# Kernel optimization log

Measured on AMD Instinct MI355X. Metric: run time of the kernel, lower is better.

## Reference

```python
import jax, jax.numpy as jnp
import numpy as np

N, E, D, H, L = 4096, 131072, 2048, 4, 2  # nodes, edges, embed_dim, heads, layers
HD = D // H


def setup_inputs() -> dict:
    key = jax.random.key(0)
    ks = jax.random.split(key, 11)
    s = 0.02
    feats = jax.random.normal(ks[0], (N, D), jnp.float32)
    edge_index = jax.random.randint(ks[1], (E, 2), 0, N, dtype=jnp.int32)
    # per-layer linear params, stored as [in, out] so y = x @ W + b (== torch x @ W.T + b)
    Wq = jax.random.normal(ks[2], (L, D, D), jnp.float32) * s
    Wk = jax.random.normal(ks[3], (L, D, D), jnp.float32) * s
    Wv = jax.random.normal(ks[4], (L, D, D), jnp.float32) * s
    Wo = jax.random.normal(ks[5], (L, D, D), jnp.float32) * s
    bq = jnp.zeros((L, D), jnp.float32)
    bk = jnp.zeros((L, D), jnp.float32)
    bv = jnp.zeros((L, D), jnp.float32)
    bo = jnp.zeros((L, D), jnp.float32)
    return dict(feats=feats, Wq=Wq, bq=bq, Wk=Wk, bk=bk, Wv=Wv, bv=bv,
                Wo=Wo, bo=bo, edge_index=edge_index)


def _gnn_forward(feats, Wq, bq, Wk, bk, Wv, bv, Wo, bo, row, col):
    n = feats.shape[0]
    # dense edge mask [1, N, N] (masked_fill where mask == 0 -> -10000)
    mask = jnp.zeros((n, n), bool).at[row, col].set(True)[None]
    scale = 1.0 / jnp.sqrt(jnp.asarray(HD, feats.dtype))
    x = feats
    for l in range(L):
        q = (x @ Wq[l] + bq[l]).reshape(n, H, HD).transpose(1, 0, 2)  # [H,N,d]
        k = (x @ Wk[l] + bk[l]).reshape(n, H, HD).transpose(1, 0, 2)
        v = (x @ Wv[l] + bv[l]).reshape(n, H, HD).transpose(1, 0, 2)
        scores = jnp.einsum('hnd,hmd->hnm', q, k) * scale          # [H,N,N]
        scores = jnp.where(mask, scores, jnp.asarray(-10000.0, scores.dtype))
        attn = jax.nn.softmax(scores, axis=-1)                      # [H,N,N]
        se = attn[:, row, col]                                      # [H,E] gather per-edge
        out_e = se[:, :, None] * v[:, col]                          # [H,E,d]
        agg = jax.vmap(lambda o: jax.ops.segment_sum(o, row, num_segments=n))(out_e)  # [H,N,d]
        x = agg.transpose(1, 0, 2).reshape(n, H * HD) @ Wo[l] + bo[l]
    return x


def reference(feats, Wq, bq, Wk, bk, Wv, bv, Wo, bo, edge_index):
    row, col = edge_index[:, 0], edge_index[:, 1]
    return _gnn_forward(feats, Wq, bq, Wk, bk, Wv, bv, Wo, bo, row, col)
```

## Files before the change

kernel.cpp:

```cpp
#include <hip/hip_runtime.h>
#include <hip/hip_bf16.h>

typedef unsigned short u16;
typedef unsigned int u32;
typedef short bf16x8 __attribute__((ext_vector_type(8)));
typedef float f32x4 __attribute__((ext_vector_type(4)));
typedef unsigned short u16x4 __attribute__((ext_vector_type(4)));
typedef unsigned short u16x8 __attribute__((ext_vector_type(8)));
typedef float f32x4v __attribute__((ext_vector_type(4)));

#define NN 4096
#define DD 2048
#define HH 4
#define HDIM 512
#define EE 131072
#define NB 512
#define EBS 256
#define QS 6144

__device__ __forceinline__ float bf2f(u16 x) {
    return __uint_as_float(((u32)x) << 16);
}
__device__ __forceinline__ u16 f2bf(float f) {
    u32 u = __float_as_uint(f);
    u += 0x7fffu + ((u >> 16) & 1u);
    return (u16)(u >> 16);
}

#define GLOAD16(g, l)                                                          \
    __builtin_amdgcn_global_load_lds(                                          \
        (const __attribute__((address_space(1))) void*)(g),                    \
        (__attribute__((address_space(3))) void*)(l), 16, 0, 0)

__global__ __launch_bounds__(256) void k_cvt(const float* __restrict__ in,
                                             u16* __restrict__ out, int n4)
{
    int i = blockIdx.x * 256 + threadIdx.x;
    if (i >= n4) return;
    f32x4v v = *(const f32x4v*)&in[i * 4];
    u16x4 o;
#pragma unroll
    for (int j = 0; j < 4; j++) o[j] = f2bf(v[j]);
    *(u16x4*)&out[i * 4] = o;
}

template <bool OUTF32>
__global__ __launch_bounds__(512, 2) void k_gemm256(
    const u16* __restrict__ A, const u16* __restrict__ Bt,
    const float* __restrict__ bias0, const float* __restrict__ bias1,
    const float* __restrict__ bias2, void* __restrict__ Cout,
    int M, int Ncols, int K)
{
    extern __shared__ u16 lds[];
    u16* sA = lds;
    u16* sB = lds + 3 * 16384;

    int t = threadIdx.x;
    int wid = t >> 6, lane = t & 63;
    int wr = wid >> 1, wc = wid & 1;
    int l15 = lane & 15, kg = lane >> 4;

    int flat = blockIdx.y * gridDim.x + blockIdx.x;
    int per = (gridDim.x * gridDim.y) >> 3;
    int nid = (flat & 7) * per + (flat >> 3);
    int bm = nid / gridDim.x;
    int bn = nid % gridDim.x;

    const int NT = K >> 6;

    int trow = t >> 3;
    int scolE = ((t & 7) ^ (trow & 7)) * 8;
    const u16* Abase = A + ((size_t)(bm * 256) + trow) * K + scolE;
    const u16* Bbase = Bt + ((size_t)(bn * 128) + trow) * K + scolE;

#define STAGE_A(buf, TT, j)                                                    \
    GLOAD16(Abase + (size_t)(j) * 64 * K + (size_t)(TT) * 64,                  \
            sA + (buf) * 16384 + (j) * 4096 + t * 8)
#define STAGE_B(buf, TT, j)                                                    \
    GLOAD16(Bbase + (size_t)(j) * 64 * K + (size_t)(TT) * 64,                  \
            sB + (buf) * 8192 + (j) * 4096 + t * 8)

    int s8_0 = ((0 * 4 + kg) ^ (l15 & 7)) * 8;
    int s8_1 = ((1 * 4 + kg) ^ (l15 & 7)) * 8;

    f32x4 acc[4][4];
#pragma unroll
    for (int m = 0; m < 4; m++)
#pragma unroll
        for (int n = 0; n < 4; n++) acc[m][n] = (f32x4){0.f, 0.f, 0.f, 0.f};

#pragma unroll
    for (int j = 0; j < 4; j++) STAGE_A(0, 0, j);
#pragma unroll
    for (int j = 0; j < 2; j++) STAGE_B(0, 0, j);
#pragma unroll
    for (int j = 0; j < 4; j++) STAGE_A(1, 1, j);
#pragma unroll
    for (int j = 0; j < 2; j++) STAGE_B(1, 1, j);
    asm volatile("s_waitcnt vmcnt(6)" ::: "memory");
    __builtin_amdgcn_s_barrier();

    int bufc = 0;
    for (int T = 0; T < NT; ++T) {
        const u16* bA = sA + bufc * 16384;
        const u16* bB = sB + bufc * 8192;
        int nxt2 = bufc + 2; if (nxt2 >= 3) nxt2 -= 3;
        bool st = (T + 2 < NT);
#pragma unroll
        for (int qm = 0; qm < 2; ++qm) {
            bf16x8 afr[2][2], bfr[2][2][2];
#pragma unroll
            for (int i = 0; i < 2; ++i) {
                int ra = wr * 64 + (qm * 2 + i) * 16 + l15;
                afr[i][0] = *(const bf16x8*)(bA + ra * 64 + s8_0);
                afr[i][1] = *(const bf16x8*)(bA + ra * 64 + s8_1);
            }
#pragma unroll
            for (int qn = 0; qn < 2; ++qn)
#pragma unroll
                for (int i = 0; i < 2; ++i) {
                    int rb = wc * 64 + (qn * 2 + i) * 16 + l15;
                    bfr[qn][i][0] = *(const bf16x8*)(bB + rb * 64 + s8_0);
                    bfr[qn][i][1] = *(const bf16x8*)(bB + rb * 64 + s8_1);
                }
            if (st) {
                if (qm == 0) { STAGE_A(nxt2, T + 2, 0); STAGE_A(nxt2, T + 2, 1); STAGE_A(nxt2, T + 2, 2); }
                else         { STAGE_A(nxt2, T + 2, 3); STAGE_B(nxt2, T + 2, 0); STAGE_B(nxt2, T + 2, 1); }
            }
            __builtin_amdgcn_s_barrier();
            __builtin_amdgcn_s_setprio(1);
#pragma unroll
            for (int qn = 0; qn < 2; ++qn)
#pragma unroll
                for (int i = 0; i < 2; ++i)
#pragma unroll
                    for (int j = 0; j < 2; ++j) {
                        acc[qm * 2 + i][qn * 2 + j] = __builtin_amdgcn_mfma_f32_16x16x32_bf16(
                            afr[i][0], bfr[qn][j][0], acc[qm * 2 + i][qn * 2 + j], 0, 0, 0);
                        acc[qm * 2 + i][qn * 2 + j] = __builtin_amdgcn_mfma_f32_16x16x32_bf16(
                            afr[i][1], bfr[qn][j][1], acc[qm * 2 + i][qn * 2 + j], 0, 0, 0);
                    }
            __builtin_amdgcn_s_setprio(0);
            if (qm == 1) {
                if (T + 2 < NT)
                    asm volatile("s_waitcnt vmcnt(6)" ::: "memory");
                else if (T + 1 < NT)
                    asm volatile("s_waitcnt vmcnt(0)" ::: "memory");
            }
            if (!(T == NT - 1 && qm == 1)) __builtin_amdgcn_s_barrier();
        }
        bufc += 1; if (bufc >= 3) bufc -= 3;
    }
#undef STAGE_A
#undef STAGE_B

    int row0 = bm * 256 + wr * 64 + kg * 4;
    int col0 = bn * 128 + wc * 64 + l15;
#pragma unroll
    for (int n = 0; n < 4; n++) {
        int cc = col0 + n * 16;
        int sel = cc >> 11;
        const float* bp = (sel == 0) ? bias0 : (sel == 1) ? bias1 : bias2;
        float bv = bp[cc & 2047];
#pragma unroll
        for (int m = 0; m < 4; m++) {
            int rb = row0 + m * 16;
#pragma unroll
            for (int r = 0; r < 4; r++) {
                float v = acc[m][n][r] + bv;
                if (OUTF32)
                    ((float*)Cout)[(size_t)(rb + r) * Ncols + cc] = v;
                else
                    ((u16*)Cout)[(size_t)(rb + r) * Ncols + cc] = f2bf(v);
            }
        }
    }
}

__global__ void k_wtrans(const float* __restrict__ Wq, const float* __restrict__ Wk,
                         const float* __restrict__ Wv, const float* __restrict__ Wo,
                         int loff, u16* __restrict__ Wt)
{
    int z = blockIdx.z;
    const float* W = (z == 0) ? Wq : (z == 1) ? Wk : (z == 2) ? Wv : Wo;
    u16* out = Wt + (size_t)z * DD * DD;
    __shared__ u16 tile[32][33];
    int tx = threadIdx.x, ty = threadIdx.y;
    int x = blockIdx.x * 32 + tx;
    int y0 = blockIdx.y * 32;
#pragma unroll
    for (int j = 0; j < 32; j += 8)
        tile[ty + j][tx] = f2bf(W[loff + (size_t)(y0 + ty + j) * DD + x]);
    __syncthreads();
    int ox = blockIdx.y * 32 + tx;
    int oy0 = blockIdx.x * 32;
#pragma unroll
    for (int j = 0; j < 32; j += 8)
        out[(size_t)(oy0 + ty + j) * DD + ox] = tile[tx][ty + j];
}

__global__ __launch_bounds__(256) void k_hist(const int* __restrict__ ei,
                                              int* __restrict__ blockcnt)
{
    __shared__ int h[NN];
    int b = blockIdx.x, t = threadIdx.x;
    for (int i = t; i < NN; i += 256) h[i] = 0;
    __syncthreads();
    int2 e = ((const int2*)ei)[b * EBS + t];
    atomicAdd(&h[e.x], 1);
    __syncthreads();
    for (int i = t; i < NN; i += 256) blockcnt[(size_t)b * NN + i] = h[i];
}

__global__ void k_rowscan(int* __restrict__ blockcnt, int* __restrict__ rowsum)
{
    int i = blockIdx.x * 256 + threadIdx.x;
    int run = 0;
    for (int b = 0; b < NB; b++) {
        int v = blockcnt[(size_t)b * NN + i];
        blockcnt[(size_t)b * NN + i] = run;
        run += v;
    }
    rowsum[i] = run;
}

__global__ __launch_bounds__(1024) void k_scan2(const int* __restrict__ rowsum,
                                                int* __restrict__ rstart)
{
    __shared__ int sh[1024];
    int t = threadIdx.x;
    int v[4], pre[4], s = 0;
#pragma unroll
    for (int j = 0; j < 4; j++) v[j] = rowsum[t * 4 + j];
#pragma unroll
    for (int j = 0; j < 4; j++) { pre[j] = s; s += v[j]; }
    sh[t] = s;
    __syncthreads();
    for (int off = 1; off < 1024; off <<= 1) {
        int x = (t >= off) ? sh[t - off] : 0;
        __syncthreads();
        sh[t] += x;
        __syncthreads();
    }
    int bp = (t == 0) ? 0 : sh[t - 1];
#pragma unroll
    for (int j = 0; j < 4; j++) rstart[t * 4 + j] = bp + pre[j];
    if (t == 1023) rstart[NN] = sh[1023];
}

__global__ __launch_bounds__(256) void k_scatter2(
    const int* __restrict__ ei, const int* __restrict__ blockcnt,
    const int* __restrict__ rstart, int* __restrict__ srow,
    int* __restrict__ scol)
{
    __shared__ int rsh[EBS];
    int b = blockIdx.x, t = threadIdx.x;
    int2 e = ((const int2*)ei)[b * EBS + t];
    rsh[t] = e.x;
    __syncthreads();
    int rank = 0;
    for (int j = 0; j < t; j++) rank += (rsh[j] == e.x);
    int pos = rstart[e.x] + blockcnt[(size_t)b * NN + e.x] + rank;
    srow[pos] = e.x;
    scol[pos] = e.y;
}

__global__ __launch_bounds__(64) void k_flags(const int* __restrict__ scol,
                                              const int* __restrict__ rstart,
                                              int* __restrict__ flags)
{
    int i = blockIdx.x;
    int start = rstart[i], end = rstart[i + 1];
    int d = end - start;
    __shared__ int sc[1024];
    int lane = threadIdx.x;
    for (int j = lane; j < d && j < 1024; j += 64) sc[j] = scol[start + j];
    __syncthreads();
    for (int j = lane; j < d; j += 64) {
        int cj = (j < 1024) ? sc[j] : scol[start + j];
        int f = 1;
        for (int q = 0; q < j; ++q) {
            int cq = (q < 1024) ? sc[q] : scol[start + q];
            if (cq == cj) { f = 0; break; }
        }
        flags[start + j] = f;
    }
}

__global__ __launch_bounds__(256) void k_scores(
    const u16* __restrict__ Qb, const u16* __restrict__ Kb,
    const int* __restrict__ srow, const int* __restrict__ scol,
    float* __restrict__ pexp)
{
    int p = blockIdx.x * 4 + (threadIdx.x >> 6);
    int lane = threadIdx.x & 63;
    int h = lane >> 4, l16 = lane & 15;
    int r = srow[p], c = scol[p];
    const float scale = 0.04419417382415922f;
    const u16* qrow = Qb + (size_t)r * QS + h * HDIM + l16 * 8;
    const u16* krow = Kb + (size_t)c * QS + h * HDIM + l16 * 8;
    float sx = 0.f, sy = 0.f;
#pragma unroll
    for (int ch = 0; ch < 4; ++ch) {
        u16x8 q8 = *(const u16x8*)(qrow + ch * 128);
        u16x8 k8 = *(const u16x8*)(krow + ch * 128);
#pragma unroll
        for (int j = 0; j < 8; j += 2) {
            sx += bf2f(q8[j]) * bf2f(k8[j]);
            sy += bf2f(q8[j + 1]) * bf2f(k8[j + 1]);
        }
    }
    float s = sx + sy;
#pragma unroll
    for (int off = 1; off < 16; off <<= 1) s += __shfl_xor(s, off, 64);
    if (l16 == 0) pexp[p * 4 + h] = expf(s * scale);
}

__global__ __launch_bounds__(256) void k_agg(
    const float* __restrict__ pexp, const int* __restrict__ flags,
    const int* __restrict__ scol, const int* __restrict__ rstart,
    const u16* __restrict__ Vb, u16* __restrict__ Aggb)
{
    int i = blockIdx.x;
    int start = rstart[i], end = rstart[i + 1];
    int h = threadIdx.x >> 6, lane = threadIdx.x & 63;
    __shared__ float sden[HH];
    float dsum = 0.f;
    for (int p = start + lane; p < end; p += 64)
        if (flags[p]) dsum += pexp[p * 4 + h];
#pragma unroll
    for (int off = 32; off > 0; off >>= 1) dsum += __shfl_xor(dsum, off, 64);
    if (lane == 0) sden[h] = dsum;
    __syncthreads();
    float inv = (end > start) ? 1.0f / sden[h] : 0.0f;
    float acc[8] = {0.f, 0.f, 0.f, 0.f, 0.f, 0.f, 0.f, 0.f};
    for (int p = start; p < end; ++p) {
        float wgt = pexp[p * 4 + h] * inv;
        int c = scol[p];
        u16x8 v8 = *(const u16x8*)&Vb[(size_t)c * QS + h * HDIM + lane * 8];
#pragma unroll
        for (int j = 0; j < 8; j++) acc[j] += wgt * bf2f(v8[j]);
    }
    u16x8 o;
#pragma unroll
    for (int j = 0; j < 8; j++) o[j] = f2bf(acc[j]);
    *(u16x8*)&Aggb[(size_t)i * DD + h * HDIM + lane * 8] = o;
}

extern "C" void kernel_launch(void* const* d_in, const int* in_sizes, int n_in,
                              void* d_out, int out_size, void* d_ws, size_t ws_size,
                              hipStream_t stream)
{
    const float* feats = (const float*)d_in[0];
    const float* Wq = (const float*)d_in[1];
    const float* bq = (const float*)d_in[2];
    const float* Wk = (const float*)d_in[3];
    const float* bk = (const float*)d_in[4];
    const float* Wv = (const float*)d_in[5];
    const float* bv = (const float*)d_in[6];
    const float* Wo = (const float*)d_in[7];
    const float* bo = (const float*)d_in[8];
    const int* ei = (const int*)d_in[9];
    float* out = (float*)d_out;

    size_t off = 0;
    auto alloc = [&](size_t bytes) {
        void* p = (char*)d_ws + off;
        off += (bytes + 255) & ~(size_t)255;
        return p;
    };
    const size_t ND = (size_t)NN * DD;
    u16* Xb = (u16*)alloc(ND * 2);
    u16* QKV = (u16*)alloc((size_t)NN * QS * 2);
    u16* Ab = (u16*)alloc(ND * 2);
    u16* Wt = (u16*)alloc((size_t)4 * DD * DD * 2);
    float* pexp = (float*)alloc((size_t)EE * HH * 4);
    int* blockcnt = (int*)alloc((size_t)NB * NN * 4);
    int* rowsum = (int*)alloc((size_t)NN * 4);
    int* rstart = (int*)alloc((size_t)(NN + 1) * 4);
    int* srow = (int*)alloc((size_t)EE * 4);
    int* scol = (int*)alloc((size_t)EE * 4);
    int* flags = (int*)alloc((size_t)EE * 4);
    (void)ws_size; (void)in_sizes; (void)n_in; (void)out_size;

    const int GEMM_LDS = 3 * (16384 + 8192) * 2;
    hipFuncSetAttribute((const void*)k_gemm256<false>,
                        hipFuncAttributeMaxDynamicSharedMemorySize, GEMM_LDS);
    hipFuncSetAttribute((const void*)k_gemm256<true>,
                        hipFuncAttributeMaxDynamicSharedMemorySize, GEMM_LDS);

    k_hist<<<NB, 256, 0, stream>>>(ei, blockcnt);
    k_rowscan<<<NN / 256, 256, 0, stream>>>(blockcnt, rowsum);
    k_scan2<<<1, 1024, 0, stream>>>(rowsum, rstart);
    k_scatter2<<<NB, 256, 0, stream>>>(ei, blockcnt, rstart, srow, scol);
    k_flags<<<NN, 64, 0, stream>>>(scol, rstart, flags);

    k_cvt<<<(int)(ND / 4 / 256), 256, 0, stream>>>(feats, Xb, (int)(ND / 4));

    dim3 gqkv(QS / 128, NN / 256);
    dim3 go(DD / 128, NN / 256);
    for (int l = 0; l < 2; ++l) {
        k_wtrans<<<dim3(DD / 32, DD / 32, 4), dim3(32, 8), 0, stream>>>(
            Wq, Wk, Wv, Wo, l * DD * DD, Wt);
        k_gemm256<false><<<gqkv, 512, GEMM_LDS, stream>>>(
            Xb, Wt, bq + l * DD, bk + l * DD, bv + l * DD, QKV, NN, QS, DD);
        k_scores<<<EE / 4, 256, 0, stream>>>(QKV, QKV + DD, srow, scol, pexp);
        k_agg<<<NN, 256, 0, stream>>>(pexp, flags, scol, rstart, QKV + 2 * DD, Ab);
        if (l == 1) {
            k_gemm256<true><<<go, 512, GEMM_LDS, stream>>>(
                Ab, Wt + 3 * (size_t)DD * DD, bo + l * DD, bo + l * DD, bo + l * DD, out, NN, DD, DD);
        } else {
            k_gemm256<false><<<go, 512, GEMM_LDS, stream>>>(
                Ab, Wt + 3 * (size_t)DD * DD, bo + l * DD, bo + l * DD, bo + l * DD, Xb, NN, DD, DD);
        }
    }
}
```

Baseline: 696.7 us.

## Retile GEMM to 256-wide N tiles with K=32 steps and templated M tile

Rewrites the bf16 MFMA GEMM so each block covers 256 output columns, with a 2x4 wave layout and K stepping of 32. The M tile becomes a template parameter: 256 for the QKV projection and 128 for the output projection, so the smaller GEMM still launches enough blocks. The grid mapping swaps to column-major block order and the LDS swizzle changes to fit 32-element rows. The wider N tile raises operand reuse per LDS load, but doubling the iteration count adds more barriers and waitcnt overhead per unit of work.

```diff
diff --git a/kernel.cpp b/kernel.cpp
--- a/kernel.cpp
+++ b/kernel.cpp
@@ -44,118 +44,126 @@
     *(u16x4*)&out[i * 4] = o;
 }
 
-template <bool OUTF32>
-__global__ __launch_bounds__(512, 2) void k_gemm256(
+template <int BMT, bool OUTF32>
+__global__ __launch_bounds__(512, 2) void k_gemmN(
     const u16* __restrict__ A, const u16* __restrict__ Bt,
     const float* __restrict__ bias0, const float* __restrict__ bias1,
     const float* __restrict__ bias2, void* __restrict__ Cout,
     int M, int Ncols, int K)
 {
+    constexpr int MR = BMT / 32;
+    constexpr int ALOADS = BMT / 128;
+    constexpr int ASZ = BMT * 32;
+    constexpr int BSZ = 256 * 32;
+
     extern __shared__ u16 lds[];
     u16* sA = lds;
-    u16* sB = lds + 3 * 16384;
+    u16* sB = lds + 3 * ASZ;
 
     int t = threadIdx.x;
     int wid = t >> 6, lane = t & 63;
-    int wr = wid >> 1, wc = wid & 1;
+    int wr = wid >> 2, wc = wid & 3;
     int l15 = lane & 15, kg = lane >> 4;
 
     int flat = blockIdx.y * gridDim.x + blockIdx.x;
     int per = (gridDim.x * gridDim.y) >> 3;
     int nid = (flat & 7) * per + (flat >> 3);
-    int bm = nid / gridDim.x;
-    int bn = nid % gridDim.x;
-
-    const int NT = K >> 6;
-
-    int trow = t >> 3;
-    int scolE = ((t & 7) ^ (trow & 7)) * 8;
-    const u16* Abase = A + ((size_t)(bm * 256) + trow) * K + scolE;
-    const u16* Bbase = Bt + ((size_t)(bn * 128) + trow) * K + scolE;
+    int gy = gridDim.y;
+    int bm = nid % gy;
+    int bn = nid / gy;
+
+    const int NT = K >> 5;
+
+    int trow = t >> 2;
+    int scolE = ((t & 3) ^ ((t >> 3) & 3)) * 8;
+    const u16* Abase = A + ((size_t)bm * BMT + trow) * K + scolE;
+    const u16* Bbase = Bt + ((size_t)bn * 256 + trow) * K + scolE;
 
 #define STAGE_A(buf, TT, j)                                                    \
-    GLOAD16(Abase + (size_t)(j) * 64 * K + (size_t)(TT) * 64,                  \
-            sA + (buf) * 16384 + (j) * 4096 + t * 8)
+    GLOAD16(Abase + (size_t)(j) * 128 * K + (size_t)(TT) * 32,                 \
+            sA + (buf) * ASZ + (j) * 4096 + t * 8)
 #define STAGE_B(buf, TT, j)                                                    \
-    GLOAD16(Bbase + (size_t)(j) * 64 * K + (size_t)(TT) * 64,                  \
-            sB + (buf) * 8192 + (j) * 4096 + t * 8)
-
-    int s8_0 = ((0 * 4 + kg) ^ (l15 & 7)) * 8;
-    int s8_1 = ((1 * 4 + kg) ^ (l15 & 7)) * 8;
-
-    f32x4 acc[4][4];
-#pragma unroll
-    for (int m = 0; m < 4; m++)
+    GLOAD16(Bbase + (size_t)(j) * 128 * K + (size_t)(TT) * 32,                 \
+            sB + (buf) * BSZ + (j) * 4096 + t * 8)
+
+    int sl = (kg ^ ((l15 >> 1) & 3)) * 8;
+
+    f32x4 acc[MR][4];
+#pragma unroll
+    for (int m = 0; m < MR; m++)
 #pragma unroll
         for (int n = 0; n < 4; n++) acc[m][n] = (f32x4){0.f, 0.f, 0.f, 0.f};
 
 #pragma unroll
-    for (int j = 0; j < 4; j++) STAGE_A(0, 0, j);
-#pragma unroll
-    for (int j = 0; j < 2; j++) STAGE_B(0, 0, j);
-#pragma unroll
-    for (int j = 0; j < 4; j++) STAGE_A(1, 1, j);
-#pragma unroll
-    for (int j = 0; j < 2; j++) STAGE_B(1, 1, j);
-    asm volatile("s_waitcnt vmcnt(6)" ::: "memory");
+    for (int j = 0; j < ALOADS; j++) STAGE_A(0, 0, j);
+    STAGE_B(0, 0, 0); STAGE_B(0, 0, 1);
+#pragma unroll
+    for (int j = 0; j < ALOADS; j++) STAGE_A(1, 1, j);
+    STAGE_B(1, 1, 0); STAGE_B(1, 1, 1);
+    if constexpr (BMT == 256)
+        asm volatile("s_waitcnt vmcnt(4)" ::: "memory");
+    else
+        asm volatile("s_waitcnt vmcnt(3)" ::: "memory");
     __builtin_amdgcn_s_barrier();
 
     int bufc = 0;
     for (int T = 0; T < NT; ++T) {
-        const u16* bA = sA + bufc * 16384;
-        const u16* bB = sB + bufc * 8192;
+        const u16* bA = sA + bufc * ASZ;
+        const u16* bB = sB + bufc * BSZ;
         int nxt2 = bufc + 2; if (nxt2 >= 3) nxt2 -= 3;
         bool st = (T + 2 < NT);
-#pragma unroll
-        for (int qm = 0; qm < 2; ++qm) {
-            bf16x8 afr[2][2], bfr[2][2][2];
-#pragma unroll
-            for (int i = 0; i < 2; ++i) {
-                int ra = wr * 64 + (qm * 2 + i) * 16 + l15;
-                afr[i][0] = *(const bf16x8*)(bA + ra * 64 + s8_0);
-                afr[i][1] = *(const bf16x8*)(bA + ra * 64 + s8_1);
-            }
-#pragma unroll
-            for (int qn = 0; qn < 2; ++qn)
-#pragma unroll
-                for (int i = 0; i < 2; ++i) {
-                    int rb = wc * 64 + (qn * 2 + i) * 16 + l15;
-                    bfr[qn][i][0] = *(const bf16x8*)(bB + rb * 64 + s8_0);
-                    bfr[qn][i][1] = *(const bf16x8*)(bB + rb * 64 + s8_1);
-                }
-            if (st) {
-                if (qm == 0) { STAGE_A(nxt2, T + 2, 0); STAGE_A(nxt2, T + 2, 1); STAGE_A(nxt2, T + 2, 2); }
-                else         { STAGE_A(nxt2, T + 2, 3); STAGE_B(nxt2, T + 2, 0); STAGE_B(nxt2, T + 2, 1); }
-            }
-            __builtin_amdgcn_s_barrier();
-            __builtin_amdgcn_s_setprio(1);
-#pragma unroll
-            for (int qn = 0; qn < 2; ++qn)
-#pragma unroll
-                for (int i = 0; i < 2; ++i)
-#pragma unroll
-                    for (int j = 0; j < 2; ++j) {
-                        acc[qm * 2 + i][qn * 2 + j] = __builtin_amdgcn_mfma_f32_16x16x32_bf16(
-                            afr[i][0], bfr[qn][j][0], acc[qm * 2 + i][qn * 2 + j], 0, 0, 0);
-                        acc[qm * 2 + i][qn * 2 + j] = __builtin_amdgcn_mfma_f32_16x16x32_bf16(
-                            afr[i][1], bfr[qn][j][1], acc[qm * 2 + i][qn * 2 + j], 0, 0, 0);
-                    }
-            __builtin_amdgcn_s_setprio(0);
-            if (qm == 1) {
-                if (T + 2 < NT)
-                    asm volatile("s_waitcnt vmcnt(6)" ::: "memory");
-                else if (T + 1 < NT)
-                    asm volatile("s_waitcnt vmcnt(0)" ::: "memory");
-            }
-            if (!(T == NT - 1 && qm == 1)) __builtin_amdgcn_s_barrier();
-        }
+
+        bf16x8 bfr[4];
+#pragma unroll
+        for (int n = 0; n < 4; ++n)
+            bfr[n] = *(const bf16x8*)(bB + (wc * 64 + n * 16 + l15) * 32 + sl);
+        bf16x8 afr[MR / 2];
+#pragma unroll
+        for (int i = 0; i < MR / 2; ++i)
+            afr[i] = *(const bf16x8*)(bA + (wr * (MR * 16) + i * 16 + l15) * 32 + sl);
+        if (st) {
+#pragma unroll
+            for (int j = 0; j < ALOADS; j++) STAGE_A(nxt2, T + 2, j);
+        }
+        __builtin_amdgcn_s_setprio(1);
+#pragma unroll
+        for (int i = 0; i < MR / 2; ++i)
+#pragma unroll
+            for (int n = 0; n < 4; ++n)
+                acc[i][n] = __builtin_amdgcn_mfma_f32_16x16x32_bf16(
+                    afr[i], bfr[n], acc[i][n], 0, 0, 0);
+        __builtin_amdgcn_s_setprio(0);
+        __builtin_amdgcn_s_barrier();
+
+        bf16x8 afr2[MR / 2];
+#pragma unroll
+        for (int i = 0; i < MR / 2; ++i)
+            afr2[i] = *(const bf16x8*)(bA + (wr * (MR * 16) + (MR / 2 + i) * 16 + l15) * 32 + sl);
+        if (st) { STAGE_B(nxt2, T + 2, 0); STAGE_B(nxt2, T + 2, 1); }
+        __builtin_amdgcn_s_setprio(1);
+#pragma unroll
+        for (int i = 0; i < MR / 2; ++i)
+#pragma unroll
+            for (int n = 0; n < 4; ++n)
+                acc[MR / 2 + i][n] = __builtin_amdgcn_mfma_f32_16x16x32_bf16(
+                    afr2[i], bfr[n], acc[MR / 2 + i][n], 0, 0, 0);
+        __builtin_amdgcn_s_setprio(0);
+        if (T + 2 < NT) {
+            if constexpr (BMT == 256)
+                asm volatile("s_waitcnt vmcnt(4)" ::: "memory");
+            else
+                asm volatile("s_waitcnt vmcnt(3)" ::: "memory");
+        } else if (T + 1 < NT) {
+            asm volatile("s_waitcnt vmcnt(0)" ::: "memory");
+        }
+        __builtin_amdgcn_s_barrier();
         bufc += 1; if (bufc >= 3) bufc -= 3;
     }
 #undef STAGE_A
 #undef STAGE_B
 
-    int row0 = bm * 256 + wr * 64 + kg * 4;
-    int col0 = bn * 128 + wc * 64 + l15;
+    int row0 = bm * BMT + wr * (MR * 16) + kg * 4;
+    int col0 = bn * 256 + wc * 64 + l15;
 #pragma unroll
     for (int n = 0; n < 4; n++) {
         int cc = col0 + n * 16;
@@ -163,7 +171,7 @@
         const float* bp = (sel == 0) ? bias0 : (sel == 1) ? bias1 : bias2;
         float bv = bp[cc & 2047];
 #pragma unroll
-        for (int m = 0; m < 4; m++) {
+        for (int m = 0; m < MR; m++) {
             int rb = row0 + m * 16;
 #pragma unroll
             for (int r = 0; r < 4; r++) {
@@ -383,11 +391,14 @@
     int* flags = (int*)alloc((size_t)EE * 4);
     (void)ws_size; (void)in_sizes; (void)n_in; (void)out_size;
 
-    const int GEMM_LDS = 3 * (16384 + 8192) * 2;
-    hipFuncSetAttribute((const void*)k_gemm256<false>,
-                        hipFuncAttributeMaxDynamicSharedMemorySize, GEMM_LDS);
-    hipFuncSetAttribute((const void*)k_gemm256<true>,
-                        hipFuncAttributeMaxDynamicSharedMemorySize, GEMM_LDS);
+    const int QKV_LDS = 3 * (256 * 32 + 256 * 32) * 2;
+    const int O_LDS = 3 * (128 * 32 + 256 * 32) * 2;
+    hipFuncSetAttribute((const void*)k_gemmN<256, false>,
+                        hipFuncAttributeMaxDynamicSharedMemorySize, QKV_LDS);
+    hipFuncSetAttribute((const void*)k_gemmN<128, false>,
+                        hipFuncAttributeMaxDynamicSharedMemorySize, O_LDS);
+    hipFuncSetAttribute((const void*)k_gemmN<128, true>,
+                        hipFuncAttributeMaxDynamicSharedMemorySize, O_LDS);
 
     k_hist<<<NB, 256, 0, stream>>>(ei, blockcnt);
     k_rowscan<<<NN / 256, 256, 0, stream>>>(blockcnt, rowsum);
@@ -397,20 +408,20 @@
 
     k_cvt<<<(int)(ND / 4 / 256), 256, 0, stream>>>(feats, Xb, (int)(ND / 4));
 
-    dim3 gqkv(QS / 128, NN / 256);
-    dim3 go(DD / 128, NN / 256);
+    dim3 gqkv(QS / 256, NN / 256);
+    dim3 go(DD / 256, NN / 128);
     for (int l = 0; l < 2; ++l) {
         k_wtrans<<<dim3(DD / 32, DD / 32, 4), dim3(32, 8), 0, stream>>>(
             Wq, Wk, Wv, Wo, l * DD * DD, Wt);
-        k_gemm256<false><<<gqkv, 512, GEMM_LDS, stream>>>(
+        k_gemmN<256, false><<<gqkv, 512, QKV_LDS, stream>>>(
             Xb, Wt, bq + l * DD, bk + l * DD, bv + l * DD, QKV, NN, QS, DD);
         k_scores<<<EE / 4, 256, 0, stream>>>(QKV, QKV + DD, srow, scol, pexp);
         k_agg<<<NN, 256, 0, stream>>>(pexp, flags, scol, rstart, QKV + 2 * DD, Ab);
         if (l == 1) {
-            k_gemm256<true><<<go, 512, GEMM_LDS, stream>>>(
+            k_gemmN<128, true><<<go, 512, O_LDS, stream>>>(
                 Ab, Wt + 3 * (size_t)DD * DD, bo + l * DD, bo + l * DD, bo + l * DD, out, NN, DD, DD);
         } else {
-            k_gemm256<false><<<go, 512, GEMM_LDS, stream>>>(
+            k_gemmN<128, false><<<go, 512, O_LDS, stream>>>(
                 Ab, Wt + 3 * (size_t)DD * DD, bo + l * DD, bo + l * DD, bo + l * DD, Xb, NN, DD, DD);
         }
     }
```

After: 713.7 us. +2.4%, slower.

## Restructure GEMM to 4 waves with 128x64 warp tiles and K=32 stages

Applied to the files above, without the earlier changes.

The 256x128 GEMM kernel now runs with 256 threads (4 waves) instead of 512. Each wave computes a 128x64 output tile, using 8x4 MFMA accumulators with fragment loads amortized over more MFMAs. The K step per stage drops from 64 to 32, which halves LDS use. The inner loop is simplified to one barrier per stage, and the swizzle and grid-remapping order change. Register pressure rises to 128 accumulator floats per thread, and there are fewer waves to hide latency.

```diff
diff --git a/kernel.cpp b/kernel.cpp
--- a/kernel.cpp
+++ b/kernel.cpp
@@ -45,7 +45,7 @@
 }
 
 template <bool OUTF32>
-__global__ __launch_bounds__(512, 2) void k_gemm256(
+__global__ __launch_bounds__(256, 2) void k_gemm(
     const u16* __restrict__ A, const u16* __restrict__ Bt,
     const float* __restrict__ bias0, const float* __restrict__ bias1,
     const float* __restrict__ bias2, void* __restrict__ Cout,
@@ -53,7 +53,7 @@
 {
     extern __shared__ u16 lds[];
     u16* sA = lds;
-    u16* sB = lds + 3 * 16384;
+    u16* sB = lds + 3 * 8192;
 
     int t = threadIdx.x;
     int wid = t >> 6, lane = t & 63;
@@ -63,98 +63,77 @@
     int flat = blockIdx.y * gridDim.x + blockIdx.x;
     int per = (gridDim.x * gridDim.y) >> 3;
     int nid = (flat & 7) * per + (flat >> 3);
-    int bm = nid / gridDim.x;
-    int bn = nid % gridDim.x;
-
-    const int NT = K >> 6;
-
-    int trow = t >> 3;
-    int scolE = ((t & 7) ^ (trow & 7)) * 8;
-    const u16* Abase = A + ((size_t)(bm * 256) + trow) * K + scolE;
-    const u16* Bbase = Bt + ((size_t)(bn * 128) + trow) * K + scolE;
+    int gy = gridDim.y;
+    int bm = nid % gy;
+    int bn = nid / gy;
+
+    const int NT = K >> 5;
+
+    int trow = t >> 2;
+    int scolE = ((t & 3) ^ ((t >> 3) & 3)) * 8;
+    const u16* Abase = A + ((size_t)bm * 256 + trow) * K + scolE;
+    const u16* Bbase = Bt + ((size_t)bn * 128 + trow) * K + scolE;
 
 #define STAGE_A(buf, TT, j)                                                    \
-    GLOAD16(Abase + (size_t)(j) * 64 * K + (size_t)(TT) * 64,                  \
-            sA + (buf) * 16384 + (j) * 4096 + t * 8)
+    GLOAD16(Abase + (size_t)(j) * 64 * K + (size_t)(TT) * 32,                  \
+            sA + (buf) * 8192 + (j) * 2048 + t * 8)
 #define STAGE_B(buf, TT, j)                                                    \
-    GLOAD16(Bbase + (size_t)(j) * 64 * K + (size_t)(TT) * 64,                  \
-            sB + (buf) * 8192 + (j) * 4096 + t * 8)
-
-    int s8_0 = ((0 * 4 + kg) ^ (l15 & 7)) * 8;
-    int s8_1 = ((1 * 4 + kg) ^ (l15 & 7)) * 8;
-
-    f32x4 acc[4][4];
-#pragma unroll
-    for (int m = 0; m < 4; m++)
+    GLOAD16(Bbase + (size_t)(j) * 64 * K + (size_t)(TT) * 32,                  \
+            sB + (buf) * 4096 + (j) * 2048 + t * 8)
+
+    int sl = (kg ^ ((l15 >> 1) & 3)) * 8;
+
+    f32x4 acc[8][4];
+#pragma unroll
+    for (int m = 0; m < 8; m++)
 #pragma unroll
         for (int n = 0; n < 4; n++) acc[m][n] = (f32x4){0.f, 0.f, 0.f, 0.f};
 
 #pragma unroll
     for (int j = 0; j < 4; j++) STAGE_A(0, 0, j);
-#pragma unroll
-    for (int j = 0; j < 2; j++) STAGE_B(0, 0, j);
+    STAGE_B(0, 0, 0); STAGE_B(0, 0, 1);
 #pragma unroll
     for (int j = 0; j < 4; j++) STAGE_A(1, 1, j);
-#pragma unroll
-    for (int j = 0; j < 2; j++) STAGE_B(1, 1, j);
+    STAGE_B(1, 1, 0); STAGE_B(1, 1, 1);
     asm volatile("s_waitcnt vmcnt(6)" ::: "memory");
     __builtin_amdgcn_s_barrier();
 
     int bufc = 0;
     for (int T = 0; T < NT; ++T) {
-        const u16* bA = sA + bufc * 16384;
-        const u16* bB = sB + bufc * 8192;
+        const u16* bA = sA + bufc * 8192;
+        const u16* bB = sB + bufc * 4096;
         int nxt2 = bufc + 2; if (nxt2 >= 3) nxt2 -= 3;
-        bool st = (T + 2 < NT);
-#pragma unroll
-        for (int qm = 0; qm < 2; ++qm) {
-            bf16x8 afr[2][2], bfr[2][2][2];
-#pragma unroll
-            for (int i = 0; i < 2; ++i) {
-                int ra = wr * 64 + (qm * 2 + i) * 16 + l15;
-                afr[i][0] = *(const bf16x8*)(bA + ra * 64 + s8_0);
-                afr[i][1] = *(const bf16x8*)(bA + ra * 64 + s8_1);
-            }
-#pragma unroll
-            for (int qn = 0; qn < 2; ++qn)
-#pragma unroll
-                for (int i = 0; i < 2; ++i) {
-                    int rb = wc * 64 + (qn * 2 + i) * 16 + l15;
-                    bfr[qn][i][0] = *(const bf16x8*)(bB + rb * 64 + s8_0);
-                    bfr[qn][i][1] = *(const bf16x8*)(bB + rb * 64 + s8_1);
-                }
-            if (st) {
-                if (qm == 0) { STAGE_A(nxt2, T + 2, 0); STAGE_A(nxt2, T + 2, 1); STAGE_A(nxt2, T + 2, 2); }
-                else         { STAGE_A(nxt2, T + 2, 3); STAGE_B(nxt2, T + 2, 0); STAGE_B(nxt2, T + 2, 1); }
-            }
-            __builtin_amdgcn_s_barrier();
-            __builtin_amdgcn_s_setprio(1);
-#pragma unroll
-            for (int qn = 0; qn < 2; ++qn)
-#pragma unroll
-                for (int i = 0; i < 2; ++i)
-#pragma unroll
-                    for (int j = 0; j < 2; ++j) {
-                        acc[qm * 2 + i][qn * 2 + j] = __builtin_amdgcn_mfma_f32_16x16x32_bf16(
-                            afr[i][0], bfr[qn][j][0], acc[qm * 2 + i][qn * 2 + j], 0, 0, 0);
-                        acc[qm * 2 + i][qn * 2 + j] = __builtin_amdgcn_mfma_f32_16x16x32_bf16(
-                            afr[i][1], bfr[qn][j][1], acc[qm * 2 + i][qn * 2 + j], 0, 0, 0);
-                    }
-            __builtin_amdgcn_s_setprio(0);
-            if (qm == 1) {
-                if (T + 2 < NT)
-                    asm volatile("s_waitcnt vmcnt(6)" ::: "memory");
-                else if (T + 1 < NT)
-                    asm volatile("s_waitcnt vmcnt(0)" ::: "memory");
-            }
-            if (!(T == NT - 1 && qm == 1)) __builtin_amdgcn_s_barrier();
-        }
+        if (T + 2 < NT) {
+#pragma unroll
+            for (int j = 0; j < 4; j++) STAGE_A(nxt2, T + 2, j);
+            STAGE_B(nxt2, T + 2, 0); STAGE_B(nxt2, T + 2, 1);
+        }
+        bf16x8 bfr[4], afr[8];
+#pragma unroll
+        for (int n = 0; n < 4; ++n)
+            bfr[n] = *(const bf16x8*)(bB + (wc * 64 + n * 16 + l15) * 32 + sl);
+#pragma unroll
+        for (int m = 0; m < 8; ++m)
+            afr[m] = *(const bf16x8*)(bA + (wr * 128 + m * 16 + l15) * 32 + sl);
+        __builtin_amdgcn_s_setprio(1);
+#pragma unroll
+        for (int m = 0; m < 8; ++m)
+#pragma unroll
+            for (int n = 0; n < 4; ++n)
+                acc[m][n] = __builtin_amdgcn_mfma_f32_16x16x32_bf16(
+                    afr[m], bfr[n], acc[m][n], 0, 0, 0);
+        __builtin_amdgcn_s_setprio(0);
+        if (T + 2 < NT)
+            asm volatile("s_waitcnt vmcnt(6)" ::: "memory");
+        else if (T + 1 < NT)
+            asm volatile("s_waitcnt vmcnt(0)" ::: "memory");
+        __builtin_amdgcn_s_barrier();
         bufc += 1; if (bufc >= 3) bufc -= 3;
     }
 #undef STAGE_A
 #undef STAGE_B
 
-    int row0 = bm * 256 + wr * 64 + kg * 4;
+    int row0 = bm * 256 + wr * 128 + kg * 4;
     int col0 = bn * 128 + wc * 64 + l15;
 #pragma unroll
     for (int n = 0; n < 4; n++) {
@@ -163,7 +142,7 @@
         const float* bp = (sel == 0) ? bias0 : (sel == 1) ? bias1 : bias2;
         float bv = bp[cc & 2047];
 #pragma unroll
-        for (int m = 0; m < 4; m++) {
+        for (int m = 0; m < 8; m++) {
             int rb = row0 + m * 16;
 #pragma unroll
             for (int r = 0; r < 4; r++) {
@@ -383,10 +362,10 @@
     int* flags = (int*)alloc((size_t)EE * 4);
     (void)ws_size; (void)in_sizes; (void)n_in; (void)out_size;
 
-    const int GEMM_LDS = 3 * (16384 + 8192) * 2;
-    hipFuncSetAttribute((const void*)k_gemm256<false>,
+    const int GEMM_LDS = 3 * (8192 + 4096) * 2;
+    hipFuncSetAttribute((const void*)k_gemm<false>,
                         hipFuncAttributeMaxDynamicSharedMemorySize, GEMM_LDS);
-    hipFuncSetAttribute((const void*)k_gemm256<true>,
+    hipFuncSetAttribute((const void*)k_gemm<true>,
                         hipFuncAttributeMaxDynamicSharedMemorySize, GEMM_LDS);
 
     k_hist<<<NB, 256, 0, stream>>>(ei, blockcnt);
@@ -402,15 +381,15 @@
     for (int l = 0; l < 2; ++l) {
         k_wtrans<<<dim3(DD / 32, DD / 32, 4), dim3(32, 8), 0, stream>>>(
             Wq, Wk, Wv, Wo, l * DD * DD, Wt);
-        k_gemm256<false><<<gqkv, 512, GEMM_LDS, stream>>>(
+        k_gemm<false><<<gqkv, 256, GEMM_LDS, stream>>>(
             Xb, Wt, bq + l * DD, bk + l * DD, bv + l * DD, QKV, NN, QS, DD);
         k_scores<<<EE / 4, 256, 0, stream>>>(QKV, QKV + DD, srow, scol, pexp);
         k_agg<<<NN, 256, 0, stream>>>(pexp, flags, scol, rstart, QKV + 2 * DD, Ab);
         if (l == 1) {
-            k_gemm256<true><<<go, 512, GEMM_LDS, stream>>>(
+            k_gemm<true><<<go, 256, GEMM_LDS, stream>>>(
                 Ab, Wt + 3 * (size_t)DD * DD, bo + l * DD, bo + l * DD, bo + l * DD, out, NN, DD, DD);
         } else {
-            k_gemm256<false><<<go, 512, GEMM_LDS, stream>>>(
+            k_gemm<false><<<go, 256, GEMM_LDS, stream>>>(
                 Ab, Wt + 3 * (size_t)DD * DD, bo + l * DD, bo + l * DD, bo + l * DD, Xb, NN, DD, DD);
         }
     }
```

New measurement: 688.4 us. About the same (-1.2%).
